# Optimization experiments

Hardware: AMD Instinct MI355X
Metric: run time of the kernel (lower is better)

The kernel has to match this reference:

```python
import jax, jax.numpy as jnp
import numpy as np

HIDDEN = 256
HEADS = 8
HEAD_DIM = HIDDEN // HEADS
SCALE = HEAD_DIM ** -0.5
N = 4096
NUM_GRAPHS = 16
LN_EPS = 1e-5


def setup_inputs() -> dict:
    key = jax.random.key(0)
    ks = jax.random.split(key, 8)
    x = jax.random.normal(ks[0], (N, HIDDEN), dtype=jnp.float32)
    batch = jnp.sort(jax.random.randint(ks[1], (N,), 0, NUM_GRAPHS, dtype=jnp.int64))
    # Xavier-uniform linear weights, stored as [in, out] (y = x @ W + b)
    lim = float(np.sqrt(6.0 / (HIDDEN + HIDDEN)))
    def W(k):
        return jax.random.uniform(k, (HIDDEN, HIDDEN), jnp.float32, -lim, lim)
    return {
        "x": x,
        "batch": batch,
        "Wq": W(ks[2]), "bq": jnp.zeros((HIDDEN,), jnp.float32),
        "Wk": W(ks[3]), "bk": jnp.zeros((HIDDEN,), jnp.float32),
        "Wv": W(ks[4]), "bv": jnp.zeros((HIDDEN,), jnp.float32),
        "Wo": W(ks[5]), "bo": jnp.zeros((HIDDEN,), jnp.float32),
        "gamma": jnp.ones((HIDDEN,), jnp.float32),
        "beta": jnp.zeros((HIDDEN,), jnp.float32),
    }


def _layer_norm(x, gamma, beta):
    mu = jnp.mean(x, axis=-1, keepdims=True)
    var = jnp.mean(jnp.square(x - mu), axis=-1, keepdims=True)
    return (x - mu) * jax.lax.rsqrt(var + LN_EPS) * gamma + beta


def reference(x, batch, Wq, bq, Wk, bk, Wv, bv, Wo, bo, gamma, beta):
    residual = x
    h = _layer_norm(x, gamma, beta)
    n = h.shape[0]
    q = (h @ Wq + bq).reshape(n, HEADS, HEAD_DIM)
    k = (h @ Wk + bk).reshape(n, HEADS, HEAD_DIM)
    v = (h @ Wv + bv).reshape(n, HEADS, HEAD_DIM)
    # dense scores masked to block-diagonal (same-graph) structure
    scores = jnp.einsum('ihd,jhd->ihj', q, k) * SCALE  # [N, H, N]
    same_graph = (batch[None, :] == batch[:, None])[:, None, :]  # [N, 1, N]
    scores = jnp.where(same_graph, scores, -jnp.inf)
    attn = jax.nn.softmax(scores, axis=-1)
    attn = jnp.nan_to_num(attn, nan=0.0)
    out = jnp.einsum('ihj,jhd->ihd', attn, v).reshape(n, HIDDEN)
    out = out @ Wo + bo
    return residual + out
```

## Files before the change

kernel.cpp:

```cpp
#include <hip/hip_runtime.h>

#define NNODES 4096
#define HID 256
#define NG 16
#define NH 8
#define HD 32
#define LN_EPS 1e-5f
#define QSCALE (0.17677669529663687f * 1.4426950408889634f)
#define CAPT 384
#define KLS 40
#define VTS (CAPT + 2)

typedef unsigned short u16;
typedef unsigned int u32;
typedef __bf16 bf16x8 __attribute__((ext_vector_type(8)));
typedef float f32x4 __attribute__((ext_vector_type(4)));

__device__ __forceinline__ float bf2f(u16 u){
  union { u32 i; float f; } c; c.i = ((u32)u) << 16; return c.f;
}
__device__ __forceinline__ u16 f2bf(float f){
  union { float f; u32 i; } c; c.f = f;
  u32 x = c.i;
  return (u16)((x + 0x7fffu + ((x >> 16) & 1u)) >> 16);
}

__global__ __launch_bounds__(256) void prep_kernel(
    const float* __restrict__ x, const float* __restrict__ gamma,
    const float* __restrict__ beta, u16* __restrict__ h,
    const float* __restrict__ Wq, const float* __restrict__ Wk,
    const float* __restrict__ Wv, const float* __restrict__ Wo,
    u16* __restrict__ Wt, const int* __restrict__ bw, int* __restrict__ seg){
  __shared__ u16 tile[32][33];
  __shared__ int bad;
  int b = blockIdx.x;
  if (b < 1024){
    int wave = threadIdx.x >> 6, lane = threadIdx.x & 63;
    int row = b * 4 + wave;
    float4 xv = ((const float4*)x)[row * 64 + lane];
    float a0 = xv.x, a1 = xv.y, a2 = xv.z, a3 = xv.w;
    float s = a0 + a1 + a2 + a3;
    #pragma unroll
    for (int m = 1; m < 64; m <<= 1) s += __shfl_xor(s, m);
    float mu = s * (1.0f / HID);
    float d0 = a0 - mu, d1 = a1 - mu, d2 = a2 - mu, d3 = a3 - mu;
    float vv = d0*d0 + d1*d1 + d2*d2 + d3*d3;
    #pragma unroll
    for (int m = 1; m < 64; m <<= 1) vv += __shfl_xor(vv, m);
    float rs = rsqrtf(vv * (1.0f / HID) + LN_EPS);
    float4 gv = ((const float4*)gamma)[lane];
    float4 bv = ((const float4*)beta)[lane];
    ushort4 o;
    o.x = f2bf(d0 * rs * gv.x + bv.x);
    o.y = f2bf(d1 * rs * gv.y + bv.y);
    o.z = f2bf(d2 * rs * gv.z + bv.z);
    o.w = f2bf(d3 * rs * gv.w + bv.w);
    *(ushort4*)(h + (size_t)row * HID + lane * 4) = o;
  } else if (b < 1280){
    int idx = b - 1024;
    int w = idx >> 6;
    int t = idx & 63;
    int bx = (t & 7) * 32, by = (t >> 3) * 32;
    const float* src = (w == 0) ? Wq : (w == 1) ? Wk : (w == 2) ? Wv : Wo;
    u16* dst = Wt + (size_t)w * HID * HID;
    int tx = threadIdx.x & 31, ty = threadIdx.x >> 5;
    #pragma unroll
    for (int r = 0; r < 32; r += 8)
      tile[ty + r][tx] = f2bf(src[(size_t)(by + ty + r) * HID + bx + tx]);
    __syncthreads();
    #pragma unroll
    for (int r = 0; r < 32; r += 8)
      dst[(size_t)(bx + ty + r) * HID + by + tx] = tile[tx][ty + r];
  } else {
    if (threadIdx.x == 0) bad = 0;
    __syncthreads();
    int local_bad = 0;
    for (int i = threadIdx.x; i < NNODES; i += 256){
      int v = bw[i];
      if (v < 0 || v > 15) local_bad = 1;
      if (i + 1 < NNODES && bw[i + 1] < v) local_bad = 1;
    }
    if (local_bad) atomicOr(&bad, 1);
    __syncthreads();
    int stride = bad ? 2 : 1;
    int g = threadIdx.x;
    if (g <= NG){
      int lo = 0, hi = NNODES;
      while (lo < hi){
        int mid = (lo + hi) >> 1;
        if (bw[mid * stride] < g) lo = mid + 1; else hi = mid;
      }
      seg[g] = lo;
    }
  }
}

template<bool FINAL>
__device__ __forceinline__ void gemm_tile(const u16* __restrict__ A, const u16* __restrict__ Bt,
    const float* __restrict__ bias, const float* __restrict__ resid, void* __restrict__ out){
  int gw = blockIdx.x * 4 + (threadIdx.x >> 6);
  int lane = threadIdx.x & 63;
  int lr = lane & 15, lq = lane >> 4;
  int m0 = (gw >> 4) * 64;
  int n0 = (gw & 15) * 16;
  f32x4 acc[4] = {};
  const u16* arow = A + (size_t)(m0 + lr) * HID + lq * 8;
  const u16* brow = Bt + (size_t)(n0 + lr) * HID + lq * 8;
  #pragma unroll
  for (int k0 = 0; k0 < HID; k0 += 32){
    bf16x8 b = *(const bf16x8*)(brow + k0);
    #pragma unroll
    for (int t = 0; t < 4; t++){
      bf16x8 a = *(const bf16x8*)(arow + (size_t)t * 16 * HID + k0);
      acc[t] = __builtin_amdgcn_mfma_f32_16x16x32_bf16(a, b, acc[t], 0, 0, 0);
    }
  }
  int col = n0 + lr;
  float bb = bias[col];
  #pragma unroll
  for (int t = 0; t < 4; t++){
    #pragma unroll
    for (int r = 0; r < 4; r++){
      int row = m0 + 16 * t + lq * 4 + r;
      float val = acc[t][r] + bb;
      if (FINAL){
        val += resid[(size_t)row * HID + col];
        ((float*)out)[(size_t)row * HID + col] = val;
      } else {
        ((u16*)out)[(size_t)row * HID + col] = f2bf(val);
      }
    }
  }
}

__global__ __launch_bounds__(256) void gemm_qkv_kernel(const u16* __restrict__ h,
    const u16* __restrict__ Wt, const float* __restrict__ bq, const float* __restrict__ bk,
    const float* __restrict__ bv, u16* __restrict__ q, u16* __restrict__ k, u16* __restrict__ v){
  int which = blockIdx.y;
  const u16* B = Wt + (size_t)which * HID * HID;
  const float* bias = (which == 0) ? bq : (which == 1) ? bk : bv;
  u16* out = (which == 0) ? q : (which == 1) ? k : v;
  gemm_tile<false>(h, B, bias, nullptr, out);
}

__global__ __launch_bounds__(256) void gemm_proj_kernel(const u16* __restrict__ ao,
    const u16* __restrict__ WtO, const float* __restrict__ bo, const float* __restrict__ x,
    float* __restrict__ out){
  gemm_tile<true>(ao, WtO, bo, x, out);
}

__global__ __launch_bounds__(512, 4) void attn_kernel(const u16* __restrict__ q,
    const u16* __restrict__ k, const u16* __restrict__ v, const int* __restrict__ seg,
    u16* __restrict__ out){
  __shared__ u16 kl[CAPT * KLS];
  __shared__ u16 vt[HD * VTS];
  __shared__ float mg[4][10][64];
  int gh = blockIdx.y;
  int g = gh >> 3, hd = gh & 7;
  int start = seg[g], end = seg[g + 1];
  int len = end - start;
  if (len <= 0) return;
  if (len > CAPT) len = CAPT;
  int ntj = (len + 15) >> 4;
  int nj16 = ntj << 4;
  for (int idx = threadIdx.x; idx < nj16 * 4; idx += 512){
    int row = idx >> 2, part = idx & 3;
    uint4 val = make_uint4(0, 0, 0, 0);
    if (row < len)
      val = *(const uint4*)&k[(size_t)(start + row) * HID + hd * HD + part * 8];
    *(uint4*)&kl[row * KLS + part * 8] = val;
  }
  for (int idx = threadIdx.x; idx < nj16 * 4; idx += 512){
    int row = idx >> 2, part = idx & 3;
    uint4 w = make_uint4(0, 0, 0, 0);
    if (row < len)
      w = *(const uint4*)&v[(size_t)(start + row) * HID + hd * HD + part * 8];
    int d0 = part * 8;
    vt[(d0 + 0) * VTS + row] = (u16)(w.x & 0xffffu);
    vt[(d0 + 1) * VTS + row] = (u16)(w.x >> 16);
    vt[(d0 + 2) * VTS + row] = (u16)(w.y & 0xffffu);
    vt[(d0 + 3) * VTS + row] = (u16)(w.y >> 16);
    vt[(d0 + 4) * VTS + row] = (u16)(w.z & 0xffffu);
    vt[(d0 + 5) * VTS + row] = (u16)(w.z >> 16);
    vt[(d0 + 6) * VTS + row] = (u16)(w.w & 0xffffu);
    vt[(d0 + 7) * VTS + row] = (u16)(w.w >> 16);
  }
  __syncthreads();
  int wave = threadIdx.x >> 6, lane = threadIdx.x & 63;
  int lq = lane >> 4, lr = lane & 15;
  int tl = wave & 3;
  int jh = wave >> 2;
  int nouter = (ntj + 15) >> 4;
  for (int it = 0; it < nouter; it++){
    int tq = it * 16 + blockIdx.x * 4 + tl;
    bool active = tq < ntj;
    int q0 = tq << 4;
    float m = -3.0e38f, l = 0.f;
    f32x4 o0 = {0.f,0.f,0.f,0.f}, o1 = {0.f,0.f,0.f,0.f};
    if (active){
      bf16x8 qf = *(const bf16x8*)&q[(size_t)(start + q0 + lr) * HID + hd * HD + lq * 8];
      int half = (ntj + 1) >> 1;
      int jt0 = jh ? half : 0;
      int jt1 = jh ? ntj : half;
      for (int jt = jt0; jt < jt1; jt++){
        int j0 = jt << 4;
        bf16x8 kf = *(const bf16x8*)&kl[(j0 + lr) * KLS + lq * 8];
        f32x4 st = __builtin_amdgcn_mfma_f32_16x16x32_bf16(kf, qf,
                     (f32x4){0.f,0.f,0.f,0.f}, 0, 0, 0);
        int jb = j0 + lq * 4;
        float s0 = (jb + 0 < len) ? st[0] * QSCALE : -3.0e38f;
        float s1 = (jb + 1 < len) ? st[1] * QSCALE : -3.0e38f;
        float s2 = (jb + 2 < len) ? st[2] * QSCALE : -3.0e38f;
        float s3 = (jb + 3 < len) ? st[3] * QSCALE : -3.0e38f;
        float tm = fmaxf(fmaxf(s0, s1), fmaxf(s2, s3));
        tm = fmaxf(tm, __shfl_xor(tm, 16));
        tm = fmaxf(tm, __shfl_xor(tm, 32));
        float mn = fmaxf(m, tm);
        float alpha = exp2f(m - mn);
        float p0 = exp2f(s0 - mn), p1 = exp2f(s1 - mn);
        float p2 = exp2f(s2 - mn), p3 = exp2f(s3 - mn);
        float ps = (p0 + p1) + (p2 + p3);
        ps += __shfl_xor(ps, 16);
        ps += __shfl_xor(ps, 32);
        l = l * alpha + ps;
        m = mn;
        union { bf16x8 v8; u32 w[4]; } pf, vf0, vf1;
        pf.w[0] = (u32)f2bf(p0) | ((u32)f2bf(p1) << 16);
        pf.w[1] = (u32)f2bf(p2) | ((u32)f2bf(p3) << 16);
        pf.w[2] = 0; pf.w[3] = 0;
        const u16* vp0 = &vt[lr * VTS + j0 + lq * 4];
        const u16* vp1 = &vt[(16 + lr) * VTS + j0 + lq * 4];
        vf0.w[0] = *(const u32*)vp0; vf0.w[1] = *(const u32*)(vp0 + 2);
        vf0.w[2] = 0; vf0.w[3] = 0;
        vf1.w[0] = *(const u32*)vp1; vf1.w[1] = *(const u32*)(vp1 + 2);
        vf1.w[2] = 0; vf1.w[3] = 0;
        o0 = o0 * alpha;
        o1 = o1 * alpha;
        o0 = __builtin_amdgcn_mfma_f32_16x16x32_bf16(vf0.v8, pf.v8, o0, 0, 0, 0);
        o1 = __builtin_amdgcn_mfma_f32_16x16x32_bf16(vf1.v8, pf.v8, o1, 0, 0, 0);
      }
    }
    if (jh == 1){
      mg[tl][0][lane] = o0[0]; mg[tl][1][lane] = o0[1];
      mg[tl][2][lane] = o0[2]; mg[tl][3][lane] = o0[3];
      mg[tl][4][lane] = o1[0]; mg[tl][5][lane] = o1[1];
      mg[tl][6][lane] = o1[2]; mg[tl][7][lane] = o1[3];
      mg[tl][8][lane] = m;     mg[tl][9][lane] = l;
    }
    __syncthreads();
    if (jh == 0 && active && q0 + lr < len){
      float m2 = mg[tl][8][lane], l2 = mg[tl][9][lane];
      float mn = fmaxf(m, m2);
      float a  = exp2f(m - mn);
      float a2 = exp2f(m2 - mn);
      float lt = l * a + l2 * a2;
      float rl = 1.0f / lt;
      float r0 = (o0[0]*a + mg[tl][0][lane]*a2) * rl;
      float r1 = (o0[1]*a + mg[tl][1][lane]*a2) * rl;
      float r2 = (o0[2]*a + mg[tl][2][lane]*a2) * rl;
      float r3 = (o0[3]*a + mg[tl][3][lane]*a2) * rl;
      float r4 = (o1[0]*a + mg[tl][4][lane]*a2) * rl;
      float r5 = (o1[1]*a + mg[tl][5][lane]*a2) * rl;
      float r6 = (o1[2]*a + mg[tl][6][lane]*a2) * rl;
      float r7 = (o1[3]*a + mg[tl][7][lane]*a2) * rl;
      u16* orow = out + (size_t)(start + q0 + lr) * HID + hd * HD;
      int dbase = lq * 4;
      *(u32*)&orow[dbase]          = (u32)f2bf(r0) | ((u32)f2bf(r1) << 16);
      *(u32*)&orow[dbase + 2]      = (u32)f2bf(r2) | ((u32)f2bf(r3) << 16);
      *(u32*)&orow[16 + dbase]     = (u32)f2bf(r4) | ((u32)f2bf(r5) << 16);
      *(u32*)&orow[16 + dbase + 2] = (u32)f2bf(r6) | ((u32)f2bf(r7) << 16);
    }
    __syncthreads();
  }
}

__global__ void sentinel_kernel(u32* __restrict__ out, int nwords){
  int i = blockIdx.x * 256 + threadIdx.x;
  if (i < nwords) out[i] = 0x46404640u;
}

extern "C" void kernel_launch(void* const* d_in, const int* in_sizes, int n_in,
                              void* d_out, int out_size, void* d_ws, size_t ws_size,
                              hipStream_t stream){
  const float* x   = (const float*)d_in[0];
  const int* batch = (const int*)d_in[1];
  const float* Wq = (const float*)d_in[2],  *bq = (const float*)d_in[3];
  const float* Wk = (const float*)d_in[4],  *bk = (const float*)d_in[5];
  const float* Wv = (const float*)d_in[6],  *bv = (const float*)d_in[7];
  const float* Wo = (const float*)d_in[8],  *bo = (const float*)d_in[9];
  const float* gamma = (const float*)d_in[10], *beta = (const float*)d_in[11];

  const size_t WT_OFF  = 1024;
  const size_t QKV_OFF = WT_OFF + 4 * HID * HID * 2;
  const size_t BUF     = (size_t)NNODES * HID * 2;
  const size_t NEED    = QKV_OFF + 4 * BUF;

  if (ws_size < NEED){
    int nwords = out_size / 2;
    sentinel_kernel<<<(nwords + 255) / 256, 256, 0, stream>>>((u32*)d_out, nwords);
    return;
  }

  char* w = (char*)d_ws;
  int* seg  = (int*)(w + 128);
  u16* Wt   = (u16*)(w + WT_OFF);
  u16* qb   = (u16*)(w + QKV_OFF);
  u16* kb   = qb + (size_t)NNODES * HID;
  u16* vb   = kb + (size_t)NNODES * HID;
  u16* ao   = vb + (size_t)NNODES * HID;
  u16* h    = (u16*)d_out;

  prep_kernel<<<1281, 256, 0, stream>>>(x, gamma, beta, h, Wq, Wk, Wv, Wo, Wt, batch, seg);
  gemm_qkv_kernel<<<dim3(256, 3), 256, 0, stream>>>(h, Wt, bq, bk, bv, qb, kb, vb);
  attn_kernel<<<dim3(4, NG * NH), 512, 0, stream>>>(qb, kb, vb, seg, ao);
  gemm_proj_kernel<<<256, 256, 0, stream>>>(ao, Wt + 3 * (size_t)HID * HID, bo, x, (float*)d_out);
}
```

Baseline: 128.7 us.

## Fuse LayerNorm into QKV GEMM and drop prep kernel

Removes the separate prep kernel. LayerNorm is recomputed per block into LDS and fed straight to the QKV MFMA GEMM. Weights are read as fp32 and converted to bf16 on the fly, with no pre-transposed copy. Graph segment bounds are found inside the attention kernel with a ballot-based search over batch. This cuts one launch and the round trip of h and Wt through memory, but each QKV block redoes the LayerNorm (12 times per row) and loads weights strided with repeated conversion.

```diff
diff --git a/kernel.cpp b/kernel.cpp
--- a/kernel.cpp
+++ b/kernel.cpp
@@ -10,154 +10,137 @@
 #define CAPT 384
 #define KLS 40
 #define VTS (CAPT + 2)
+#define HLS 264
 
 typedef unsigned short u16;
 typedef unsigned int u32;
 typedef __bf16 bf16x8 __attribute__((ext_vector_type(8)));
 typedef float f32x4 __attribute__((ext_vector_type(4)));
 
-__device__ __forceinline__ float bf2f(u16 u){
-  union { u32 i; float f; } c; c.i = ((u32)u) << 16; return c.f;
-}
 __device__ __forceinline__ u16 f2bf(float f){
   union { float f; u32 i; } c; c.f = f;
   u32 x = c.i;
   return (u16)((x + 0x7fffu + ((x >> 16) & 1u)) >> 16);
 }
 
-__global__ __launch_bounds__(256) void prep_kernel(
+__global__ __launch_bounds__(256) void lnqkv_kernel(
     const float* __restrict__ x, const float* __restrict__ gamma,
-    const float* __restrict__ beta, u16* __restrict__ h,
+    const float* __restrict__ beta,
     const float* __restrict__ Wq, const float* __restrict__ Wk,
-    const float* __restrict__ Wv, const float* __restrict__ Wo,
-    u16* __restrict__ Wt, const int* __restrict__ bw, int* __restrict__ seg){
-  __shared__ u16 tile[32][33];
-  __shared__ int bad;
-  int b = blockIdx.x;
-  if (b < 1024){
-    int wave = threadIdx.x >> 6, lane = threadIdx.x & 63;
-    int row = b * 4 + wave;
-    float4 xv = ((const float4*)x)[row * 64 + lane];
-    float a0 = xv.x, a1 = xv.y, a2 = xv.z, a3 = xv.w;
-    float s = a0 + a1 + a2 + a3;
-    #pragma unroll
-    for (int m = 1; m < 64; m <<= 1) s += __shfl_xor(s, m);
+    const float* __restrict__ Wv,
+    const float* __restrict__ bq, const float* __restrict__ bk,
+    const float* __restrict__ bv,
+    u16* __restrict__ qb, u16* __restrict__ kb, u16* __restrict__ vb){
+  __shared__ u16 hl[64][HLS];
+  int bid = blockIdx.x;
+  int which = blockIdx.y;
+  int wave = threadIdx.x >> 6, lane = threadIdx.x & 63;
+  int m0 = (bid >> 2) * 64;
+  int nb = (bid & 3) * 64 + wave * 16;
+  const float* W    = (which == 0) ? Wq : (which == 1) ? Wk : Wv;
+  const float* bias = (which == 0) ? bq : (which == 1) ? bk : bv;
+  u16* out          = (which == 0) ? qb : (which == 1) ? kb : vb;
+
+  int rsub = lane >> 4;
+  int c16  = lane & 15;
+  float4 g0 = *(const float4*)(gamma + c16 * 16 + 0);
+  float4 g1 = *(const float4*)(gamma + c16 * 16 + 4);
+  float4 g2 = *(const float4*)(gamma + c16 * 16 + 8);
+  float4 g3 = *(const float4*)(gamma + c16 * 16 + 12);
+  float4 t0 = *(const float4*)(beta + c16 * 16 + 0);
+  float4 t1 = *(const float4*)(beta + c16 * 16 + 4);
+  float4 t2 = *(const float4*)(beta + c16 * 16 + 8);
+  float4 t3 = *(const float4*)(beta + c16 * 16 + 12);
+  float ga[16] = {g0.x,g0.y,g0.z,g0.w, g1.x,g1.y,g1.z,g1.w,
+                  g2.x,g2.y,g2.z,g2.w, g3.x,g3.y,g3.z,g3.w};
+  float bt[16] = {t0.x,t0.y,t0.z,t0.w, t1.x,t1.y,t1.z,t1.w,
+                  t2.x,t2.y,t2.z,t2.w, t3.x,t3.y,t3.z,t3.w};
+  #pragma unroll
+  for (int b = 0; b < 4; b++){
+    int rloc = wave * 16 + b * 4 + rsub;
+    const float* xr = x + (size_t)(m0 + rloc) * HID + c16 * 16;
+    float4 v0 = *(const float4*)(xr + 0);
+    float4 v1 = *(const float4*)(xr + 4);
+    float4 v2 = *(const float4*)(xr + 8);
+    float4 v3 = *(const float4*)(xr + 12);
+    float e[16] = {v0.x,v0.y,v0.z,v0.w, v1.x,v1.y,v1.z,v1.w,
+                   v2.x,v2.y,v2.z,v2.w, v3.x,v3.y,v3.z,v3.w};
+    float s = 0.f;
+    #pragma unroll
+    for (int i = 0; i < 16; i++) s += e[i];
+    s += __shfl_xor(s, 1); s += __shfl_xor(s, 2);
+    s += __shfl_xor(s, 4); s += __shfl_xor(s, 8);
     float mu = s * (1.0f / HID);
-    float d0 = a0 - mu, d1 = a1 - mu, d2 = a2 - mu, d3 = a3 - mu;
-    float vv = d0*d0 + d1*d1 + d2*d2 + d3*d3;
-    #pragma unroll
-    for (int m = 1; m < 64; m <<= 1) vv += __shfl_xor(vv, m);
+    float vv = 0.f;
+    #pragma unroll
+    for (int i = 0; i < 16; i++){ e[i] -= mu; vv += e[i] * e[i]; }
+    vv += __shfl_xor(vv, 1); vv += __shfl_xor(vv, 2);
+    vv += __shfl_xor(vv, 4); vv += __shfl_xor(vv, 8);
     float rs = rsqrtf(vv * (1.0f / HID) + LN_EPS);
-    float4 gv = ((const float4*)gamma)[lane];
-    float4 bv = ((const float4*)beta)[lane];
-    ushort4 o;
-    o.x = f2bf(d0 * rs * gv.x + bv.x);
-    o.y = f2bf(d1 * rs * gv.y + bv.y);
-    o.z = f2bf(d2 * rs * gv.z + bv.z);
-    o.w = f2bf(d3 * rs * gv.w + bv.w);
-    *(ushort4*)(h + (size_t)row * HID + lane * 4) = o;
-  } else if (b < 1280){
-    int idx = b - 1024;
-    int w = idx >> 6;
-    int t = idx & 63;
-    int bx = (t & 7) * 32, by = (t >> 3) * 32;
-    const float* src = (w == 0) ? Wq : (w == 1) ? Wk : (w == 2) ? Wv : Wo;
-    u16* dst = Wt + (size_t)w * HID * HID;
-    int tx = threadIdx.x & 31, ty = threadIdx.x >> 5;
-    #pragma unroll
-    for (int r = 0; r < 32; r += 8)
-      tile[ty + r][tx] = f2bf(src[(size_t)(by + ty + r) * HID + bx + tx]);
-    __syncthreads();
-    #pragma unroll
-    for (int r = 0; r < 32; r += 8)
-      dst[(size_t)(bx + ty + r) * HID + by + tx] = tile[tx][ty + r];
-  } else {
-    if (threadIdx.x == 0) bad = 0;
-    __syncthreads();
-    int local_bad = 0;
-    for (int i = threadIdx.x; i < NNODES; i += 256){
-      int v = bw[i];
-      if (v < 0 || v > 15) local_bad = 1;
-      if (i + 1 < NNODES && bw[i + 1] < v) local_bad = 1;
-    }
-    if (local_bad) atomicOr(&bad, 1);
-    __syncthreads();
-    int stride = bad ? 2 : 1;
-    int g = threadIdx.x;
-    if (g <= NG){
-      int lo = 0, hi = NNODES;
-      while (lo < hi){
-        int mid = (lo + hi) >> 1;
-        if (bw[mid * stride] < g) lo = mid + 1; else hi = mid;
-      }
-      seg[g] = lo;
-    }
-  }
-}
-
-template<bool FINAL>
-__device__ __forceinline__ void gemm_tile(const u16* __restrict__ A, const u16* __restrict__ Bt,
-    const float* __restrict__ bias, const float* __restrict__ resid, void* __restrict__ out){
-  int gw = blockIdx.x * 4 + (threadIdx.x >> 6);
-  int lane = threadIdx.x & 63;
+    u32 pk[8];
+    #pragma unroll
+    for (int i = 0; i < 8; i++){
+      float o0 = e[2*i]     * rs * ga[2*i]     + bt[2*i];
+      float o1 = e[2*i + 1] * rs * ga[2*i + 1] + bt[2*i + 1];
+      pk[i] = (u32)f2bf(o0) | ((u32)f2bf(o1) << 16);
+    }
+    *(uint4*)&hl[rloc][c16 * 16]     = make_uint4(pk[0], pk[1], pk[2], pk[3]);
+    *(uint4*)&hl[rloc][c16 * 16 + 8] = make_uint4(pk[4], pk[5], pk[6], pk[7]);
+  }
+  __syncthreads();
+
   int lr = lane & 15, lq = lane >> 4;
-  int m0 = (gw >> 4) * 64;
-  int n0 = (gw & 15) * 16;
   f32x4 acc[4] = {};
-  const u16* arow = A + (size_t)(m0 + lr) * HID + lq * 8;
-  const u16* brow = Bt + (size_t)(n0 + lr) * HID + lq * 8;
+  const float* wbase = W + nb + lr;
   #pragma unroll
   for (int k0 = 0; k0 < HID; k0 += 32){
-    bf16x8 b = *(const bf16x8*)(brow + k0);
+    union { bf16x8 v; u16 e[8]; } bf;
+    const float* wp = wbase + (size_t)(k0 + lq * 8) * HID;
+    #pragma unroll
+    for (int j = 0; j < 8; j++) bf.e[j] = f2bf(wp[(size_t)j * HID]);
     #pragma unroll
     for (int t = 0; t < 4; t++){
-      bf16x8 a = *(const bf16x8*)(arow + (size_t)t * 16 * HID + k0);
-      acc[t] = __builtin_amdgcn_mfma_f32_16x16x32_bf16(a, b, acc[t], 0, 0, 0);
-    }
-  }
-  int col = n0 + lr;
+      bf16x8 a = *(const bf16x8*)&hl[t * 16 + lr][k0 + lq * 8];
+      acc[t] = __builtin_amdgcn_mfma_f32_16x16x32_bf16(a, bf.v, acc[t], 0, 0, 0);
+    }
+  }
+  int col = nb + lr;
   float bb = bias[col];
   #pragma unroll
   for (int t = 0; t < 4; t++){
     #pragma unroll
     for (int r = 0; r < 4; r++){
       int row = m0 + 16 * t + lq * 4 + r;
-      float val = acc[t][r] + bb;
-      if (FINAL){
-        val += resid[(size_t)row * HID + col];
-        ((float*)out)[(size_t)row * HID + col] = val;
-      } else {
-        ((u16*)out)[(size_t)row * HID + col] = f2bf(val);
-      }
-    }
-  }
-}
-
-__global__ __launch_bounds__(256) void gemm_qkv_kernel(const u16* __restrict__ h,
-    const u16* __restrict__ Wt, const float* __restrict__ bq, const float* __restrict__ bk,
-    const float* __restrict__ bv, u16* __restrict__ q, u16* __restrict__ k, u16* __restrict__ v){
-  int which = blockIdx.y;
-  const u16* B = Wt + (size_t)which * HID * HID;
-  const float* bias = (which == 0) ? bq : (which == 1) ? bk : bv;
-  u16* out = (which == 0) ? q : (which == 1) ? k : v;
-  gemm_tile<false>(h, B, bias, nullptr, out);
-}
-
-__global__ __launch_bounds__(256) void gemm_proj_kernel(const u16* __restrict__ ao,
-    const u16* __restrict__ WtO, const float* __restrict__ bo, const float* __restrict__ x,
-    float* __restrict__ out){
-  gemm_tile<true>(ao, WtO, bo, x, out);
+      out[(size_t)row * HID + col] = f2bf(acc[t][r] + bb);
+    }
+  }
 }
 
 __global__ __launch_bounds__(512, 4) void attn_kernel(const u16* __restrict__ q,
-    const u16* __restrict__ k, const u16* __restrict__ v, const int* __restrict__ seg,
-    u16* __restrict__ out){
+    const u16* __restrict__ k, const u16* __restrict__ v,
+    const int* __restrict__ batch, int bstride, u16* __restrict__ out){
   __shared__ u16 kl[CAPT * KLS];
   __shared__ u16 vt[HD * VTS];
   __shared__ float mg[4][10][64];
+  __shared__ int s_se[2];
   int gh = blockIdx.y;
   int g = gh >> 3, hd = gh & 7;
-  int start = seg[g], end = seg[g + 1];
+  int wave = threadIdx.x >> 6, lane = threadIdx.x & 63;
+  if (wave < 2){
+    int target = g + wave;
+    int p = batch[(size_t)(lane * 64) * bstride];
+    int c = __popcll(__ballot(p < target));
+    int lo = 0;
+    if (c > 0){
+      int base = (c - 1) * 64 + 1;
+      int idx = base + lane;
+      int val = (idx < NNODES) ? batch[(size_t)idx * bstride] : 0x7fffffff;
+      lo = base + __popcll(__ballot(val < target));
+    }
+    if (lane == 0) s_se[wave] = lo;
+  }
+  __syncthreads();
+  int start = s_se[0], end = s_se[1];
   int len = end - start;
   if (len <= 0) return;
   if (len > CAPT) len = CAPT;
@@ -186,7 +169,6 @@
     vt[(d0 + 7) * VTS + row] = (u16)(w.w >> 16);
   }
   __syncthreads();
-  int wave = threadIdx.x >> 6, lane = threadIdx.x & 63;
   int lq = lane >> 4, lr = lane & 15;
   int tl = wave & 3;
   int jh = wave >> 2;
@@ -274,6 +256,41 @@
   }
 }
 
+__global__ __launch_bounds__(256) void proj_kernel(const u16* __restrict__ ao,
+    const float* __restrict__ Wo, const float* __restrict__ bo,
+    const float* __restrict__ x, float* __restrict__ out){
+  int gw = blockIdx.x * 4 + (threadIdx.x >> 6);
+  int lane = threadIdx.x & 63;
+  int lr = lane & 15, lq = lane >> 4;
+  int m0 = (gw >> 4) * 64;
+  int n0 = (gw & 15) * 16;
+  f32x4 acc[4] = {};
+  const u16* arow = ao + (size_t)(m0 + lr) * HID + lq * 8;
+  const float* wbase = Wo + n0 + lr;
+  #pragma unroll
+  for (int k0 = 0; k0 < HID; k0 += 32){
+    union { bf16x8 v; u16 e[8]; } bf;
+    const float* wp = wbase + (size_t)(k0 + lq * 8) * HID;
+    #pragma unroll
+    for (int j = 0; j < 8; j++) bf.e[j] = f2bf(wp[(size_t)j * HID]);
+    #pragma unroll
+    for (int t = 0; t < 4; t++){
+      bf16x8 a = *(const bf16x8*)(arow + (size_t)t * 16 * HID + k0);
+      acc[t] = __builtin_amdgcn_mfma_f32_16x16x32_bf16(a, bf.v, acc[t], 0, 0, 0);
+    }
+  }
+  int col = n0 + lr;
+  float bb = bo[col];
+  #pragma unroll
+  for (int t = 0; t < 4; t++){
+    #pragma unroll
+    for (int r = 0; r < 4; r++){
+      size_t row = (size_t)(m0 + 16 * t + lq * 4 + r) * HID + col;
+      out[row] = acc[t][r] + bb + x[row];
+    }
+  }
+}
+
 __global__ void sentinel_kernel(u32* __restrict__ out, int nwords){
   int i = blockIdx.x * 256 + threadIdx.x;
   if (i < nwords) out[i] = 0x46404640u;
@@ -290,10 +307,8 @@
   const float* Wo = (const float*)d_in[8],  *bo = (const float*)d_in[9];
   const float* gamma = (const float*)d_in[10], *beta = (const float*)d_in[11];
 
-  const size_t WT_OFF  = 1024;
-  const size_t QKV_OFF = WT_OFF + 4 * HID * HID * 2;
-  const size_t BUF     = (size_t)NNODES * HID * 2;
-  const size_t NEED    = QKV_OFF + 4 * BUF;
+  const size_t BUF  = (size_t)NNODES * HID * 2;
+  const size_t NEED = 1024 + 4 * BUF;
 
   if (ws_size < NEED){
     int nwords = out_size / 2;
@@ -301,17 +316,16 @@
     return;
   }
 
+  int bstride = (in_sizes[1] >= NNODES * 8) ? 2 : 1;
+
   char* w = (char*)d_ws;
-  int* seg  = (int*)(w + 128);
-  u16* Wt   = (u16*)(w + WT_OFF);
-  u16* qb   = (u16*)(w + QKV_OFF);
-  u16* kb   = qb + (size_t)NNODES * HID;
-  u16* vb   = kb + (size_t)NNODES * HID;
-  u16* ao   = vb + (size_t)NNODES * HID;
-  u16* h    = (u16*)d_out;
-
-  prep_kernel<<<1281, 256, 0, stream>>>(x, gamma, beta, h, Wq, Wk, Wv, Wo, Wt, batch, seg);
-  gemm_qkv_kernel<<<dim3(256, 3), 256, 0, stream>>>(h, Wt, bq, bk, bv, qb, kb, vb);
-  attn_kernel<<<dim3(4, NG * NH), 512, 0, stream>>>(qb, kb, vb, seg, ao);
-  gemm_proj_kernel<<<256, 256, 0, stream>>>(ao, Wt + 3 * (size_t)HID * HID, bo, x, (float*)d_out);
-}
+  u16* qb = (u16*)(w + 1024);
+  u16* kb = qb + (size_t)NNODES * HID;
+  u16* vb = kb + (size_t)NNODES * HID;
+  u16* ao = vb + (size_t)NNODES * HID;
+
+  lnqkv_kernel<<<dim3(256, 3), 256, 0, stream>>>(x, gamma, beta, Wq, Wk, Wv,
+                                                 bq, bk, bv, qb, kb, vb);
+  attn_kernel<<<dim3(4, NG * NH), 512, 0, stream>>>(qb, kb, vb, batch, bstride, ao);
+  proj_kernel<<<256, 256, 0, stream>>>(ao, Wo, bo, x, (float*)d_out);
+}
```

Result: faster. 115.8 us (-10.0%).
